# Kernel tuning notes

Measured on AMD Instinct MI355X. Metric: run time of the kernel, lower is better.

## Reference

```python
import jax, jax.numpy as jnp
import numpy as np

TEMPERATURE = 0.5


def setup_inputs() -> dict:
    key = jax.random.key(0)
    k1, k2 = jax.random.split(key)
    B, D = 4096, 256
    emb_i = jax.random.normal(k1, (B, D), dtype=jnp.float32)
    emb_j = jax.random.normal(k2, (B, D), dtype=jnp.float32)
    return {"emb_i": emb_i, "emb_j": emb_j}


def reference(emb_i, emb_j):
    B = emb_i.shape[0]
    # L2-normalize along feature dim (torch F.normalize uses eps=1e-12 clamp)
    def l2norm(x):
        n = jnp.sqrt(jnp.sum(x * x, axis=1, keepdims=True))
        return x / jnp.maximum(n, 1e-12)

    z_i = l2norm(emb_i)
    z_j = l2norm(emb_j)
    reps = jnp.concatenate([z_i, z_j], axis=0)  # [2B, D]
    # cosine similarity of normalized rows == plain GEMM
    sim = (reps @ reps.T) / TEMPERATURE  # [2B, 2B]
    # mask out self-similarity on the diagonal
    diag = jnp.eye(2 * B, dtype=bool)
    sim = jnp.where(diag, -jnp.inf, sim)
    # labels: row i -> i+B, row B+i -> i
    labels = jnp.concatenate([jnp.arange(B) + B, jnp.arange(B)])
    logp = jax.nn.log_softmax(sim, axis=1)
    loss = -jnp.mean(jnp.take_along_axis(logp, labels[:, None], axis=1))
    return loss
```

## Files before the change

### kernel.cpp

```cpp
#include <hip/hip_runtime.h>

typedef int i32x4 __attribute__((ext_vector_type(4)));
typedef float f32x4 __attribute__((ext_vector_type(4)));

#define D_DIM 256
#define C2 2.88539008f
#define LN2 0.69314718f

__global__ __launch_bounds__(256) void k_normalize(const float* __restrict__ ei,
                                                   const float* __restrict__ ej,
                                                   unsigned char* __restrict__ R,
                                                   unsigned* __restrict__ ticket,
                                                   int B) {
  if (blockIdx.x == 0 && threadIdx.x == 0) *ticket = 0u;
  const int w = threadIdx.x >> 6, lane = threadIdx.x & 63;
  const int row = blockIdx.x * 16 + w * 4 + (lane >> 4);
  const int kq = lane & 15;
  const float* src = (row < B) ? (ei + (size_t)row * D_DIM)
                               : (ej + (size_t)(row - B) * D_DIM);
  const float4* s4 = (const float4*)src + kq * 4;
  float4 v0 = s4[0], v1 = s4[1], v2 = s4[2], v3 = s4[3];
  float ss = v0.x*v0.x + v0.y*v0.y + v0.z*v0.z + v0.w*v0.w
           + v1.x*v1.x + v1.y*v1.y + v1.z*v1.z + v1.w*v1.w
           + v2.x*v2.x + v2.y*v2.y + v2.z*v2.z + v2.w*v2.w
           + v3.x*v3.x + v3.y*v3.y + v3.z*v3.z + v3.w*v3.w;
#pragma unroll
  for (int d = 1; d < 16; d <<= 1) ss += __shfl_xor(ss, d, 64);
  const float s = 1.0f / fmaxf(sqrtf(ss), 1e-12f);
  int q0 = __builtin_amdgcn_cvt_pk_fp8_f32(v0.x*s, v0.y*s, 0, 0);
  q0     = __builtin_amdgcn_cvt_pk_fp8_f32(v0.z*s, v0.w*s, q0, 1);
  int q1 = __builtin_amdgcn_cvt_pk_fp8_f32(v1.x*s, v1.y*s, 0, 0);
  q1     = __builtin_amdgcn_cvt_pk_fp8_f32(v1.z*s, v1.w*s, q1, 1);
  int q2 = __builtin_amdgcn_cvt_pk_fp8_f32(v2.x*s, v2.y*s, 0, 0);
  q2     = __builtin_amdgcn_cvt_pk_fp8_f32(v2.z*s, v2.w*s, q2, 1);
  int q3 = __builtin_amdgcn_cvt_pk_fp8_f32(v3.x*s, v3.y*s, 0, 0);
  q3     = __builtin_amdgcn_cvt_pk_fp8_f32(v3.z*s, v3.w*s, q3, 1);
  i32x4 o = {q0, q1, q2, q3};
  ((i32x4*)R)[(size_t)row * 16 + kq] = o;
}

__global__ __launch_bounds__(256, 4) void k_simgemm(const unsigned char* __restrict__ R,
                                                    float* __restrict__ rowPartial,
                                                    float* __restrict__ simTgt,
                                                    int N) {
  __shared__ char lds[2][16 * 1024];
  const int tid = threadIdx.x;
  const int w = tid >> 6, lane = tid & 63;
  const int wr = w >> 1, wc = w & 1;
  const int half = N >> 1;

  const int T = N / 128;
  const int t = blockIdx.x;
  int bi = (int)(((float)(2 * T + 1) -
                  sqrtf((float)((2 * T + 1) * (2 * T + 1) - 8 * t))) * 0.5f);
  while (bi > 0 && t < bi * (2 * T - bi + 1) / 2) --bi;
  while (t >= (bi + 1) * (2 * T - bi) / 2) ++bi;
  const int bj = bi + (t - bi * (2 * T - bi + 1) / 2);
  const int brow = bi * 128, bcol = bj * 128;
  const bool offdiag = (bi != bj);

  f32x4 acc[4][4];
#pragma unroll
  for (int m = 0; m < 4; ++m)
#pragma unroll
    for (int n = 0; n < 4; ++n) acc[m][n] = (f32x4){0.f, 0.f, 0.f, 0.f};

  auto stage = [&](int buf, int kt) {
    char* dst = lds[buf];
#pragma unroll
    for (int i = 0; i < 4; ++i) {
      const int cid = i * 256 + tid;
      const int panel = cid >> 9;
      const int pc = cid & 511;
      const int r = pc >> 2, cs = pc & 3;
      const int c = cs ^ ((r >> 1) & 3);
      const unsigned char* g =
          R + (size_t)((panel ? bcol : brow) + r) * 256 + kt * 64 + c * 16;
      __builtin_amdgcn_global_load_lds(
          (const __attribute__((address_space(1))) void*)g,
          (__attribute__((address_space(3))) void*)(dst + (size_t)cid * 16), 16, 0, 0);
    }
  };

  auto compute = [&](int buf) {
    const char* ldsA = lds[buf];
    const char* ldsB = lds[buf] + 8 * 1024;
    const int g = lane >> 4, c15 = lane & 15;
    long a[4][2], b[4][2];
#pragma unroll
    for (int m = 0; m < 4; ++m) {
      const int row = wr * 64 + m * 16 + c15;
      const int sw = (row >> 1) & 3;
#pragma unroll
      for (int ks = 0; ks < 2; ++ks) {
        const int chunk = (ks * 2 + (g >> 1)) ^ sw;
        a[m][ks] = *(const long*)(ldsA + row * 64 + chunk * 16 + (g & 1) * 8);
      }
    }
#pragma unroll
    for (int n = 0; n < 4; ++n) {
      const int col = wc * 64 + n * 16 + c15;
      const int sw = (col >> 1) & 3;
#pragma unroll
      for (int ks = 0; ks < 2; ++ks) {
        const int chunk = (ks * 2 + (g >> 1)) ^ sw;
        b[n][ks] = *(const long*)(ldsB + col * 64 + chunk * 16 + (g & 1) * 8);
      }
    }
#pragma unroll
    for (int ks = 0; ks < 2; ++ks)
#pragma unroll
      for (int m = 0; m < 4; ++m)
#pragma unroll
        for (int n = 0; n < 4; ++n)
          acc[m][n] = __builtin_amdgcn_mfma_f32_16x16x32_fp8_fp8(
              a[m][ks], b[n][ks], acc[m][n], 0, 0, 0);
  };

  stage(0, 0);
#pragma unroll
  for (int kt = 0; kt < 4; ++kt) {
    const int cur = kt & 1;
    if (kt < 3) {
      stage(cur ^ 1, kt + 1);
      asm volatile("s_waitcnt vmcnt(4)" ::: "memory");
    } else {
      asm volatile("s_waitcnt vmcnt(0)" ::: "memory");
    }
    __builtin_amdgcn_s_barrier();
    compute(cur);
    __builtin_amdgcn_s_barrier();
  }

  float cs4[4] = {0.f, 0.f, 0.f, 0.f};
#pragma unroll
  for (int m = 0; m < 4; ++m) {
#pragma unroll
    for (int j = 0; j < 4; ++j) {
      const int gr = brow + wr * 64 + m * 16 + (lane >> 4) * 4 + j;
      const int tgt = (gr < half) ? gr + half : gr - half;
      float rs = 0.f;
#pragma unroll
      for (int n = 0; n < 4; ++n) {
        const int gc = bcol + wc * 64 + n * 16 + (lane & 15);
        const float sv2 = acc[m][n][j] * C2;
        const float ev = (gr == gc) ? 0.f : __builtin_amdgcn_exp2f(sv2);
        if (gc == tgt) {
          simTgt[gr] = sv2;
          if (offdiag) simTgt[gc] = sv2;
        }
        rs += ev;
        cs4[n] += ev;
      }
#pragma unroll
      for (int d = 1; d < 16; d <<= 1) rs += __shfl_xor(rs, d, 64);
      if ((lane & 15) == 0)
        rowPartial[(size_t)(bj * 2 + wc) * N + gr] = rs;
    }
  }
  if (offdiag) {
#pragma unroll
    for (int n = 0; n < 4; ++n) {
      float c = cs4[n];
      c += __shfl_xor(c, 16, 64);
      c += __shfl_xor(c, 32, 64);
      if ((lane >> 4) == 0)
        rowPartial[(size_t)(bi * 2 + wr) * N + (bcol + wc * 64 + n * 16 + lane)] = c;
    }
  }
}

__global__ __launch_bounds__(256) void k_rowreduce(const float* __restrict__ rowPartial,
                                                   const float* __restrict__ simTgt,
                                                   float* __restrict__ blockOut,
                                                   unsigned* __restrict__ ticket,
                                                   float* __restrict__ out, int N) {
  const int lane = threadIdx.x & 63;
  const int q = threadIdx.x >> 6;
  const int row = blockIdx.x * 64 + lane;
  float part = 0.f;
#pragma unroll 8
  for (int c = q * 32; c < q * 32 + 32; ++c)
    part += rowPartial[(size_t)c * N + row];
  __shared__ float red[4][64];
  __shared__ int isLast;
  red[q][lane] = part;
  __syncthreads();
  if (threadIdx.x < 64) {
    const float denom = red[0][lane] + red[1][lane] + red[2][lane] + red[3][lane];
    float lossr = (__builtin_amdgcn_logf(denom) - simTgt[row]) * LN2;
#pragma unroll
    for (int d = 32; d; d >>= 1) lossr += __shfl_xor(lossr, d, 64);
    if (threadIdx.x == 0) {
      atomicExch(&blockOut[blockIdx.x], lossr);
      isLast = (atomicAdd(ticket, 1u) == gridDim.x - 1);
    }
  }
  __syncthreads();
  if (isLast && threadIdx.x < 64) {
    float v = atomicAdd(&blockOut[threadIdx.x], 0.0f) +
              atomicAdd(&blockOut[64 + threadIdx.x], 0.0f);
#pragma unroll
    for (int d = 32; d; d >>= 1) v += __shfl_xor(v, d, 64);
    if (threadIdx.x == 0) out[0] = v / (float)N;
  }
}

extern "C" void kernel_launch(void* const* d_in, const int* in_sizes, int n_in,
                              void* d_out, int out_size, void* d_ws, size_t ws_size,
                              hipStream_t stream) {
  const float* ei = (const float*)d_in[0];
  const float* ej = (const float*)d_in[1];
  const int B = in_sizes[0] / D_DIM;
  const int N = 2 * B;

  char* ws = (char*)d_ws;
  unsigned char* R = (unsigned char*)ws;
  float* rowPartial = (float*)(ws + (size_t)N * D_DIM);
  float* simTgt     = (float*)(ws + (size_t)N * D_DIM + (size_t)128 * N * 4);
  float* blockOut   = (float*)((char*)simTgt + (size_t)N * 4);
  unsigned* ticket  = (unsigned*)((char*)blockOut + 128 * 4);

  k_normalize<<<N / 16, 256, 0, stream>>>(ei, ej, R, ticket, B);
  const int T = N / 128;
  k_simgemm<<<T * (T + 1) / 2, 256, 0, stream>>>(R, rowPartial, simTgt, N);
  k_rowreduce<<<N / 64, 256, 0, stream>>>(rowPartial, simTgt, blockOut, ticket,
                                          (float*)d_out, N);
}
```

Measured before the change: 44.29 us.

## Accumulate row denominators with atomics and replace row-reduce with single-block final

The GEMM epilogue now adds its row and column partial exp-sums straight into a per-row denominator array with float atomics, instead of writing a 128-by-N partial matrix that a separate kernel later re-reads. The multi-block row-reduce kernel and its ticket-based last-block logic are replaced by one 1024-thread block that computes log(denom) minus target and sums it. This removes the 4 MB partial-matrix write and read. In exchange it adds atomic contention on each row (up to 128 adds per row), makes the summation order nondeterministic, and runs the final reduction serially in one block, whose loop assumes N is 8192.

```diff
diff --git a/kernel.cpp b/kernel.cpp
--- a/kernel.cpp
+++ b/kernel.cpp
@@ -10,9 +10,9 @@
 __global__ __launch_bounds__(256) void k_normalize(const float* __restrict__ ei,
                                                    const float* __restrict__ ej,
                                                    unsigned char* __restrict__ R,
-                                                   unsigned* __restrict__ ticket,
+                                                   float* __restrict__ denom,
                                                    int B) {
-  if (blockIdx.x == 0 && threadIdx.x == 0) *ticket = 0u;
+  if (threadIdx.x < 16) denom[blockIdx.x * 16 + threadIdx.x] = 0.f;
   const int w = threadIdx.x >> 6, lane = threadIdx.x & 63;
   const int row = blockIdx.x * 16 + w * 4 + (lane >> 4);
   const int kq = lane & 15;
@@ -40,7 +40,7 @@
 }
 
 __global__ __launch_bounds__(256, 4) void k_simgemm(const unsigned char* __restrict__ R,
-                                                    float* __restrict__ rowPartial,
+                                                    float* __restrict__ denom,
                                                     float* __restrict__ simTgt,
                                                     int N) {
   __shared__ char lds[2][16 * 1024];
@@ -154,8 +154,7 @@
       }
 #pragma unroll
       for (int d = 1; d < 16; d <<= 1) rs += __shfl_xor(rs, d, 64);
-      if ((lane & 15) == 0)
-        rowPartial[(size_t)(bj * 2 + wc) * N + gr] = rs;
+      if ((lane & 15) == 0) atomicAdd(&denom[gr], rs);
     }
   }
   if (offdiag) {
@@ -165,43 +164,29 @@
       c += __shfl_xor(c, 16, 64);
       c += __shfl_xor(c, 32, 64);
       if ((lane >> 4) == 0)
-        rowPartial[(size_t)(bi * 2 + wr) * N + (bcol + wc * 64 + n * 16 + lane)] = c;
-    }
-  }
-}
-
-__global__ __launch_bounds__(256) void k_rowreduce(const float* __restrict__ rowPartial,
-                                                   const float* __restrict__ simTgt,
-                                                   float* __restrict__ blockOut,
-                                                   unsigned* __restrict__ ticket,
-                                                   float* __restrict__ out, int N) {
-  const int lane = threadIdx.x & 63;
-  const int q = threadIdx.x >> 6;
-  const int row = blockIdx.x * 64 + lane;
-  float part = 0.f;
-#pragma unroll 8
-  for (int c = q * 32; c < q * 32 + 32; ++c)
-    part += rowPartial[(size_t)c * N + row];
-  __shared__ float red[4][64];
-  __shared__ int isLast;
-  red[q][lane] = part;
+        atomicAdd(&denom[bcol + wc * 64 + n * 16 + (lane & 15)], c);
+    }
+  }
+}
+
+__global__ __launch_bounds__(1024) void k_final(const float* __restrict__ denom,
+                                                const float* __restrict__ simTgt,
+                                                float* __restrict__ out, int N) {
+  float acc = 0.f;
+#pragma unroll
+  for (int i = 0; i < 8; ++i) {
+    const int row = i * 1024 + threadIdx.x;
+    acc += (__builtin_amdgcn_logf(denom[row]) - simTgt[row]) * LN2;
+  }
+#pragma unroll
+  for (int d = 32; d; d >>= 1) acc += __shfl_xor(acc, d, 64);
+  __shared__ float red[16];
+  if ((threadIdx.x & 63) == 0) red[threadIdx.x >> 6] = acc;
   __syncthreads();
   if (threadIdx.x < 64) {
-    const float denom = red[0][lane] + red[1][lane] + red[2][lane] + red[3][lane];
-    float lossr = (__builtin_amdgcn_logf(denom) - simTgt[row]) * LN2;
-#pragma unroll
-    for (int d = 32; d; d >>= 1) lossr += __shfl_xor(lossr, d, 64);
-    if (threadIdx.x == 0) {
-      atomicExch(&blockOut[blockIdx.x], lossr);
-      isLast = (atomicAdd(ticket, 1u) == gridDim.x - 1);
-    }
-  }
-  __syncthreads();
-  if (isLast && threadIdx.x < 64) {
-    float v = atomicAdd(&blockOut[threadIdx.x], 0.0f) +
-              atomicAdd(&blockOut[64 + threadIdx.x], 0.0f);
-#pragma unroll
-    for (int d = 32; d; d >>= 1) v += __shfl_xor(v, d, 64);
+    float v = (threadIdx.x < 16) ? red[threadIdx.x] : 0.f;
+#pragma unroll
+    for (int d = 8; d; d >>= 1) v += __shfl_xor(v, d, 64);
     if (threadIdx.x == 0) out[0] = v / (float)N;
   }
 }
@@ -216,14 +201,11 @@
 
   char* ws = (char*)d_ws;
   unsigned char* R = (unsigned char*)ws;
-  float* rowPartial = (float*)(ws + (size_t)N * D_DIM);
-  float* simTgt     = (float*)(ws + (size_t)N * D_DIM + (size_t)128 * N * 4);
-  float* blockOut   = (float*)((char*)simTgt + (size_t)N * 4);
-  unsigned* ticket  = (unsigned*)((char*)blockOut + 128 * 4);
-
-  k_normalize<<<N / 16, 256, 0, stream>>>(ei, ej, R, ticket, B);
+  float* denom  = (float*)(ws + (size_t)N * D_DIM);
+  float* simTgt = (float*)(ws + (size_t)N * D_DIM + (size_t)N * 4);
+
+  k_normalize<<<N / 16, 256, 0, stream>>>(ei, ej, R, denom, B);
   const int T = N / 128;
-  k_simgemm<<<T * (T + 1) / 2, 256, 0, stream>>>(R, rowPartial, simTgt, N);
-  k_rowreduce<<<N / 64, 256, 0, stream>>>(rowPartial, simTgt, blockOut, ticket,
-                                          (float*)d_out, N);
-}
+  k_simgemm<<<T * (T + 1) / 2, 256, 0, stream>>>(R, denom, simTgt, N);
+  k_final<<<1, 1024, 0, stream>>>(denom, simTgt, (float*)d_out, N);
+}
```

Measured after the change: 49.72 us. 1.12x slower.
